# Kernel optimization log

Hardware: AMD Instinct MI355X
Metric: run time of the kernel (lower is better)

## Reference

```python
import jax, jax.numpy as jnp
import numpy as np

B, C, H, W = 8, 256, 64, 64
R = 16  # reduction
D = C // R  # qk dim = 16


def setup_inputs() -> dict:
    key = jax.random.key(0)
    ks = jax.random.split(key, 6)
    s = 1.0 / np.sqrt(C)
    return {
        "x": jax.random.normal(ks[0], (B, C, H, W), jnp.float32),
        "Wq": jax.random.normal(ks[1], (D, C), jnp.float32) * s,
        "bq": jnp.zeros((D,), jnp.float32),
        "Wk": jax.random.normal(ks[2], (D, C), jnp.float32) * s,
        "bk": jnp.zeros((D,), jnp.float32),
        "Wv": jax.random.normal(ks[3], (C, C), jnp.float32) * s,
        "bv": jnp.zeros((C,), jnp.float32),
        "Wo": jax.random.normal(ks[4], (C, C), jnp.float32) * s,
        "bo": jnp.zeros((C,), jnp.float32),
        "gamma": jnp.ones((1,), jnp.float32) * 0.1,
    }


def reference(x, Wq, bq, Wk, bk, Wv, bv, Wo, bo, gamma):
    b, c, h, w = x.shape
    n = h * w
    d = Wq.shape[0]
    scale = d ** (-0.5)
    xf = x.reshape(b, c, n)                                  # [B,C,N]
    # 1x1 convs == channelwise linear projections
    q = jnp.einsum('dc,bcn->bnd', Wq, xf) + bq               # [B,N,D] (query permuted)
    k = jnp.einsum('dc,bcn->bdn', Wk, xf) + bk[:, None]      # [B,D,N]
    v = jnp.einsum('ec,bcn->ben', Wv, xf) + bv[:, None]      # [B,C,N]
    attn = jnp.einsum('bnd,bdm->bnm', q, k) * scale          # [B,N,N]
    attn = jnp.clip(attn, -50.0, 50.0)
    attn = jax.nn.softmax(attn, axis=-1)
    out = jnp.einsum('ben,bmn->bem', v, attn)                # value @ attn^T -> [B,C,N]
    out = jnp.einsum('fc,bcn->bfn', Wo, out) + bo[:, None]   # conv_out
    out = out.reshape(b, c, h, w)
    g = jnp.clip(gamma, 0.0, 1.0)
    return g[0] * out + x
```

## Files before the change

kernel.cpp:

```cpp
#include <hip/hip_runtime.h>
#include <hip/hip_bf16.h>

#define DEVI __device__ __forceinline__

using f32x4  = __attribute__((ext_vector_type(4))) float;
using s16x8  = __attribute__((ext_vector_type(8))) short;
using bf16x8 = __attribute__((ext_vector_type(8))) __bf16;

constexpr int kB = 8;
constexpr int kC = 256;
constexpr int kN = 4096;
constexpr int kD = 16;

DEVI unsigned short f2bf(float f) {
  __hip_bfloat16 h = __float2bfloat16(f);
  return __builtin_bit_cast(unsigned short, h);
}
DEVI s16x8 ld16g(const unsigned short* p) { return *reinterpret_cast<const s16x8*>(p); }
DEVI s16x8 ld16l(const char* b, int off) { return *reinterpret_cast<const s16x8*>(b + off); }
DEVI void  st16l(char* b, int off, s16x8 v) { *reinterpret_cast<s16x8*>(b + off) = v; }
DEVI f32x4 mfma16(s16x8 a, s16x8 bb, f32x4 c) {
  return __builtin_amdgcn_mfma_f32_16x16x32_bf16(
      __builtin_bit_cast(bf16x8, a), __builtin_bit_cast(bf16x8, bb), c, 0, 0, 0);
}
DEVI void gload_lds16(const void* g, void* l) {
  __builtin_amdgcn_global_load_lds((const __attribute__((address_space(1))) void*)g,
                                   (__attribute__((address_space(3))) void*)l, 16, 0, 0);
}

__global__ __launch_bounds__(256) void k_cvt_w(
    const float* wq, const float* wk, const float* wv, const float* wo,
    unsigned short* wqb, unsigned short* wkb, unsigned short* wvb, unsigned short* wob) {
  int i = blockIdx.x * 256 + threadIdx.x;
  if (i < 4096)        wqb[i]         = f2bf(wq[i]);
  else if (i < 8192)   wkb[i - 4096]  = f2bf(wk[i - 4096]);
  else if (i < 73728)  wvb[i - 8192]  = f2bf(wv[i - 8192]);
  else if (i < 139264) wob[i - 73728] = f2bf(wo[i - 73728]);
}

__global__ __launch_bounds__(256) void k_xpose(const float* __restrict__ x,
                                               unsigned short* __restrict__ xbT) {
  __shared__ float tile[64][68];
  int b = blockIdx.z, c0 = blockIdx.y * 64, n0 = blockIdx.x * 64;
  int t = threadIdx.x;
  const float* xp = x + ((size_t)b * kC + c0) * kN + n0;
#pragma unroll
  for (int i = 0; i < 4; i++) {
    int c_l = (t >> 4) + i * 16, n_l = (t & 15) * 4;
    float4 v = *reinterpret_cast<const float4*>(xp + (size_t)c_l * kN + n_l);
    *reinterpret_cast<float4*>(&tile[c_l][n_l]) = v;
  }
  __syncthreads();
  unsigned short* op = xbT + ((size_t)b * kN + n0) * kC + c0;
#pragma unroll
  for (int i = 0; i < 4; i++) {
    int n_l = (t >> 4) + i * 16, c_l = (t & 15) * 4;
    ushort4 u;
    u.x = f2bf(tile[c_l + 0][n_l]);
    u.y = f2bf(tile[c_l + 1][n_l]);
    u.z = f2bf(tile[c_l + 2][n_l]);
    u.w = f2bf(tile[c_l + 3][n_l]);
    *reinterpret_cast<ushort4*>(op + (size_t)n_l * kC + c_l) = u;
  }
}

__global__ __launch_bounds__(256) void k_proj_qkv(
    const unsigned short* __restrict__ xbT,
    const unsigned short* __restrict__ wqb, const unsigned short* __restrict__ wkb,
    const unsigned short* __restrict__ wvb,
    const float* __restrict__ bq, const float* __restrict__ bk, const float* __restrict__ bv,
    unsigned short* __restrict__ qb, unsigned short* __restrict__ kb,
    unsigned short* __restrict__ vt) {
  __shared__ char xlds[64 * 512];
  int b = blockIdx.y, n0 = blockIdx.x * 64;
  int t = threadIdx.x, lane = t & 63, w = t >> 6;
  int r = lane & 15, g = lane >> 4;
  const unsigned short* xp = xbT + ((size_t)b * kN + n0) * kC;
#pragma unroll
  for (int i = 0; i < 8; i++) {
    int ch = i * 256 + t;
    int n_l = ch >> 5, c8 = (ch & 31) << 3;
    s16x8 v = ld16g(xp + (size_t)n_l * kC + c8);
    int off = (n_l << 9) + (c8 << 1);
    off ^= (n_l & 7) << 4;
    st16l(xlds, off, v);
  }
  __syncthreads();
  {
    f32x4 aq = {0.f, 0.f, 0.f, 0.f}, ak = {0.f, 0.f, 0.f, 0.f};
#pragma unroll
    for (int kt2 = 0; kt2 < 8; kt2++) {
      int arow = w * 16 + r;
      int off = (arow << 9) + ((kt2 * 32 + g * 8) << 1);
      off ^= (arow & 7) << 4;
      s16x8 a = ld16l(xlds, off);
      s16x8 bqf = ld16g(wqb + r * kC + kt2 * 32 + g * 8);
      s16x8 bkf = ld16g(wkb + r * kC + kt2 * 32 + g * 8);
      aq = mfma16(a, bqf, aq);
      ak = mfma16(a, bkf, ak);
    }
    int d = r;
    float bqd = bq[d], bkd = bk[d];
    unsigned short* qo = qb + ((size_t)b * kN + n0 + w * 16) * kD + d;
    unsigned short* ko = kb + ((size_t)b * kN + n0 + w * 16) * kD + d;
#pragma unroll
    for (int j = 0; j < 4; j++) {
      int row = g * 4 + j;
      qo[row * kD] = f2bf((aq[j] + bqd) * 0.25f);
      ko[row * kD] = f2bf(ak[j] + bkd);
    }
  }
  {
    f32x4 acc[4][4];
#pragma unroll
    for (int p = 0; p < 4; p++)
#pragma unroll
      for (int np = 0; np < 4; np++) acc[p][np] = f32x4{0.f, 0.f, 0.f, 0.f};
#pragma unroll
    for (int kt2 = 0; kt2 < 8; kt2++) {
      s16x8 af[4], bf_[4];
#pragma unroll
      for (int p = 0; p < 4; p++) {
        int e = w * 64 + p * 16 + r;
        af[p] = ld16g(wvb + (size_t)e * kC + kt2 * 32 + g * 8);
      }
#pragma unroll
      for (int np = 0; np < 4; np++) {
        int nrow = np * 16 + r;
        int off = (nrow << 9) + ((kt2 * 32 + g * 8) << 1);
        off ^= (nrow & 7) << 4;
        bf_[np] = ld16l(xlds, off);
      }
#pragma unroll
      for (int p = 0; p < 4; p++)
#pragma unroll
        for (int np = 0; np < 4; np++) acc[p][np] = mfma16(af[p], bf_[np], acc[p][np]);
    }
#pragma unroll
    for (int p = 0; p < 4; p++) {
#pragma unroll
      for (int j = 0; j < 4; j++) {
        int e = w * 64 + p * 16 + g * 4 + j;
        float bve = bv[e];
        unsigned short* vo = vt + ((size_t)b * kC + e) * kN + n0;
#pragma unroll
        for (int np = 0; np < 4; np++) vo[np * 16 + r] = f2bf(acc[p][np][j] + bve);
      }
    }
  }
}

__global__ __launch_bounds__(256) void k_attn(
    const unsigned short* __restrict__ qb, const unsigned short* __restrict__ kb,
    const unsigned short* __restrict__ vt, const unsigned short* __restrict__ wob,
    const float* __restrict__ bo, const float* __restrict__ gamma,
    const float* __restrict__ x, float* __restrict__ out) {
  __shared__ char smem[73728];
  char* plds = smem + 65536;
  int b = blockIdx.x & 7, q0 = (blockIdx.x >> 3) * 64;
  int t = threadIdx.x, lane = t & 63, w = t >> 6;
  int r = lane & 15, g = lane >> 4;
  const s16x8 z8 = {0, 0, 0, 0, 0, 0, 0, 0};
  s16x8 qf = z8;
  if (g < 2) qf = ld16g(qb + ((size_t)b * kN + q0 + w * 16 + r) * kD + g * 8);
  f32x4 accO[16];
#pragma unroll
  for (int i = 0; i < 16; i++) accO[i] = f32x4{0.f, 0.f, 0.f, 0.f};
  float m = -1e30f, lsum = 0.f;
  const unsigned short* vbase = vt + (size_t)b * kC * kN;
  const unsigned short* kbase = kb + (size_t)b * kN * kD;

  int voff[8];
#pragma unroll
  for (int i = 0; i < 8; i++) {
    int ch = (w * 8 + i) * 64 + lane;
    int e = ch >> 3, kc = ch & 7;
    voff[i] = e * kN + (kc ^ (e & 7)) * 8;
  }
  int koff[4];
#pragma unroll
  for (int nk = 0; nk < 4; nk++) koff[nk] = (nk * 16 + r) * kD + g * 8;

  auto stage_v = [&](int key0, char* buf) {
#pragma unroll
    for (int i = 0; i < 8; i++)
      gload_lds16(vbase + voff[i] + key0, buf + (w * 8 + i) * 1024);
  };

  stage_v(0, smem);
  s16x8 kf_cur[4] = {z8, z8, z8, z8};
  if (g < 2)
#pragma unroll
    for (int nk = 0; nk < 4; nk++) kf_cur[nk] = ld16g(kbase + koff[nk]);

  for (int kt = 0; kt < kN / 64; kt++) {
    char* vbuf = smem + ((kt & 1) << 15);
    __syncthreads();
    if (kt + 1 < kN / 64) stage_v((kt + 1) * 64, smem + (((kt + 1) & 1) << 15));
    s16x8 kf_nxt[4] = {z8, z8, z8, z8};
    if (kt + 1 < kN / 64 && g < 2)
#pragma unroll
      for (int nk = 0; nk < 4; nk++)
        kf_nxt[nk] = ld16g(kbase + (kt + 1) * 64 * kD + koff[nk]);

    f32x4 s[4];
#pragma unroll
    for (int nk = 0; nk < 4; nk++) {
      f32x4 z = {0.f, 0.f, 0.f, 0.f};
      s[nk] = mfma16(kf_cur[nk], qf, z);
    }
#pragma unroll
    for (int nk = 0; nk < 4; nk++)
#pragma unroll
      for (int j = 0; j < 4; j++) s[nk][j] = fminf(50.f, fmaxf(-50.f, s[nk][j]));
    float mx0 = fmaxf(fmaxf(s[0][0], s[0][1]), fmaxf(s[0][2], s[0][3]));
    float mx1 = fmaxf(fmaxf(s[1][0], s[1][1]), fmaxf(s[1][2], s[1][3]));
    float mx2 = fmaxf(fmaxf(s[2][0], s[2][1]), fmaxf(s[2][2], s[2][3]));
    float mx3 = fmaxf(fmaxf(s[3][0], s[3][1]), fmaxf(s[3][2], s[3][3]));
    float mx = fmaxf(fmaxf(mx0, mx1), fmaxf(mx2, mx3));
    mx = fmaxf(mx, __shfl_xor(mx, 16));
    mx = fmaxf(mx, __shfl_xor(mx, 32));
    float mn = fmaxf(m, mx);
    float fs = __expf(m - mn);
    bool need = (mn != m);
    m = mn;
#pragma unroll
    for (int nk = 0; nk < 4; nk++)
#pragma unroll
      for (int j = 0; j < 4; j++) s[nk][j] = __expf(s[nk][j] - mn);
    float sm0 = (s[0][0] + s[0][1]) + (s[0][2] + s[0][3]);
    float sm1 = (s[1][0] + s[1][1]) + (s[1][2] + s[1][3]);
    float sm2 = (s[2][0] + s[2][1]) + (s[2][2] + s[2][3]);
    float sm3 = (s[3][0] + s[3][1]) + (s[3][2] + s[3][3]);
    lsum = lsum * fs + ((sm0 + sm1) + (sm2 + sm3));
#pragma unroll
    for (int nk = 0; nk < 4; nk++) {
      unsigned p01 = (unsigned)f2bf(s[nk][0]) | ((unsigned)f2bf(s[nk][1]) << 16);
      unsigned p23 = (unsigned)f2bf(s[nk][2]) | ((unsigned)f2bf(s[nk][3]) << 16);
      int off = (r << 7) + ((nk * 32 + g * 8) ^ ((r & 7) << 4));
      *reinterpret_cast<uint2*>(plds + w * 2048 + off) = make_uint2(p01, p23);
    }
    if (__any(need)) {
#pragma unroll
      for (int ep = 0; ep < 16; ep++)
#pragma unroll
        for (int j = 0; j < 4; j++) accO[ep][j] *= fs;
    }
    s16x8 pa[2];
#pragma unroll
    for (int h = 0; h < 2; h++) {
      int off = (r << 7) + ((h * 64 + g * 16) ^ ((r & 7) << 4));
      pa[h] = ld16l(plds + w * 2048, off);
    }
    __builtin_amdgcn_s_setprio(1);
#pragma unroll
    for (int ep = 0; ep < 16; ep++) {
#pragma unroll
      for (int h = 0; h < 2; h++) {
        int e = ep * 16 + r;
        int off = (e << 7) + ((h * 64 + g * 16) ^ ((e & 7) << 4));
        s16x8 vb = ld16l(vbuf, off);
        accO[ep] = mfma16(vb, pa[h], accO[ep]);
      }
    }
    __builtin_amdgcn_s_setprio(0);
#pragma unroll
    for (int nk = 0; nk < 4; nk++) kf_cur[nk] = kf_nxt[nk];
  }
  lsum += __shfl_xor(lsum, 16);
  lsum += __shfl_xor(lsum, 32);
  float inv = 1.f / lsum;
  __syncthreads();
  char* alds = smem;
#pragma unroll
  for (int ep = 0; ep < 16; ep++)
#pragma unroll
    for (int j = 0; j < 4; j++) {
      int qrow = w * 16 + r;
      int e = ep * 16 + g * 4 + j;
      int off = (qrow << 9) + ((e << 1) ^ ((qrow & 7) << 4));
      *reinterpret_cast<unsigned short*>(alds + off) = f2bf(accO[ep][j] * inv);
    }
  __syncthreads();
  f32x4 acc2[4][4];
#pragma unroll
  for (int p = 0; p < 4; p++)
#pragma unroll
    for (int np = 0; np < 4; np++) acc2[p][np] = f32x4{0.f, 0.f, 0.f, 0.f};
#pragma unroll
  for (int kt2 = 0; kt2 < 8; kt2++) {
    s16x8 af[4], bf_[4];
#pragma unroll
    for (int p = 0; p < 4; p++) {
      int f = w * 64 + p * 16 + r;
      af[p] = ld16g(wob + (size_t)f * kC + kt2 * 32 + g * 8);
    }
#pragma unroll
    for (int np = 0; np < 4; np++) {
      int mrow = np * 16 + r;
      int off = (mrow << 9) + (((kt2 * 32 + g * 8) << 1) ^ ((mrow & 7) << 4));
      bf_[np] = ld16l(alds, off);
    }
#pragma unroll
    for (int p = 0; p < 4; p++)
#pragma unroll
      for (int np = 0; np < 4; np++) acc2[p][np] = mfma16(af[p], bf_[np], acc2[p][np]);
  }
  float gm = fminf(1.f, fmaxf(0.f, gamma[0]));
#pragma unroll
  for (int p = 0; p < 4; p++) {
#pragma unroll
    for (int j = 0; j < 4; j++) {
      int f = w * 64 + p * 16 + g * 4 + j;
      float bof = bo[f];
      const float* xr = x + ((size_t)b * kC + f) * kN + q0;
      float* orow = out + ((size_t)b * kC + f) * kN + q0;
#pragma unroll
      for (int np = 0; np < 4; np++) {
        int mi = np * 16 + r;
        orow[mi] = gm * (acc2[p][np][j] + bof) + xr[mi];
      }
    }
  }
}

extern "C" void kernel_launch(void* const* d_in, const int* in_sizes, int n_in,
                              void* d_out, int out_size, void* d_ws, size_t ws_size,
                              hipStream_t stream) {
  const float* x     = (const float*)d_in[0];
  const float* Wq    = (const float*)d_in[1];
  const float* bq    = (const float*)d_in[2];
  const float* Wk    = (const float*)d_in[3];
  const float* bk    = (const float*)d_in[4];
  const float* Wv    = (const float*)d_in[5];
  const float* bv    = (const float*)d_in[6];
  const float* Wo    = (const float*)d_in[7];
  const float* bo    = (const float*)d_in[8];
  const float* gamma = (const float*)d_in[9];
  float* out = (float*)d_out;

  unsigned short* xbT = (unsigned short*)d_out;

  char* ws = (char*)d_ws;
  unsigned short* vtb = (unsigned short*)ws; ws += (size_t)kB * kC * kN * 2;
  unsigned short* qb  = (unsigned short*)ws; ws += (size_t)kB * kN * kD * 2;
  unsigned short* kbp = (unsigned short*)ws; ws += (size_t)kB * kN * kD * 2;
  unsigned short* wqb = (unsigned short*)ws; ws += kD * kC * 2;
  unsigned short* wkb = (unsigned short*)ws; ws += kD * kC * 2;
  unsigned short* wvb = (unsigned short*)ws; ws += kC * kC * 2;
  unsigned short* wob = (unsigned short*)ws; ws += kC * kC * 2;

  k_cvt_w<<<dim3(544), dim3(256), 0, stream>>>(Wq, Wk, Wv, Wo, wqb, wkb, wvb, wob);
  k_xpose<<<dim3(kN / 64, kC / 64, kB), dim3(256), 0, stream>>>(x, xbT);
  k_proj_qkv<<<dim3(kN / 64, kB), dim3(256), 0, stream>>>(xbT, wqb, wkb, wvb,
                                                          bq, bk, bv, qb, kbp, vtb);
  k_attn<<<dim3(kN / 64 * kB), dim3(256), 0, stream>>>(qb, kbp, vtb, wob,
                                                       bo, gamma, x, out);
}
```

Baseline: 253.9 us.

## Drop online softmax max with fixed exp2 offset and re-split PV work across waves

Folds log2(e) into the Q scale and replaces the running-max online softmax with a fixed offset (MFMA accumulator initialised to -kM) and clamped exp2. This removes the per-tile max reduction, shuffles and accumulator rescaling. It relies on the score clip at ±50 so the exponentials cannot overflow. The PV stage is also re-partitioned: each wave now owns 64 output channels across all 64 queries instead of 16 queries across all channels. That needs an extra barrier per tile to share P through LDS and per-row inverse sums in LDS. Packed bf16 conversion instructions replace the scalar conversions.

```diff
diff --git a/kernel.cpp b/kernel.cpp
--- a/kernel.cpp
+++ b/kernel.cpp
@@ -12,9 +12,20 @@
 constexpr int kN = 4096;
 constexpr int kD = 16;
 
+#if __has_builtin(__builtin_amdgcn_exp2f)
+#define EXP2(x) __builtin_amdgcn_exp2f(x)
+#else
+#define EXP2(x) exp2f(x)
+#endif
+
 DEVI unsigned short f2bf(float f) {
   __hip_bfloat16 h = __float2bfloat16(f);
   return __builtin_bit_cast(unsigned short, h);
+}
+DEVI unsigned cvtpk(float lo, float hi) {
+  unsigned r;
+  asm("v_cvt_pk_bf16_f32 %0, %1, %2" : "=v"(r) : "v"(lo), "v"(hi));
+  return r;
 }
 DEVI s16x8 ld16g(const unsigned short* p) { return *reinterpret_cast<const s16x8*>(p); }
 DEVI s16x8 ld16l(const char* b, int off) { return *reinterpret_cast<const s16x8*>(b + off); }
@@ -106,7 +117,7 @@
 #pragma unroll
     for (int j = 0; j < 4; j++) {
       int row = g * 4 + j;
-      qo[row * kD] = f2bf((aq[j] + bqd) * 0.25f);
+      qo[row * kD] = f2bf((aq[j] + bqd) * 0.3606737602f);
       ko[row * kD] = f2bf(ak[j] + bkd);
     }
   }
@@ -155,18 +166,26 @@
     const unsigned short* __restrict__ vt, const unsigned short* __restrict__ wob,
     const float* __restrict__ bo, const float* __restrict__ gamma,
     const float* __restrict__ x, float* __restrict__ out) {
-  __shared__ char smem[73728];
+  __shared__ char smem[73984];
   char* plds = smem + 65536;
+  float* linv = reinterpret_cast<float*>(smem + 73728);
   int b = blockIdx.x & 7, q0 = (blockIdx.x >> 3) * 64;
   int t = threadIdx.x, lane = t & 63, w = t >> 6;
   int r = lane & 15, g = lane >> 4;
   const s16x8 z8 = {0, 0, 0, 0, 0, 0, 0, 0};
+  constexpr int NT = kN / 64;
+  constexpr float kM  = 17.3123405f;
+  constexpr float kLo = -89.4470925f;
+  constexpr float kHi = 54.8224115f;
+
   s16x8 qf = z8;
   if (g < 2) qf = ld16g(qb + ((size_t)b * kN + q0 + w * 16 + r) * kD + g * 8);
-  f32x4 accO[16];
-#pragma unroll
-  for (int i = 0; i < 16; i++) accO[i] = f32x4{0.f, 0.f, 0.f, 0.f};
-  float m = -1e30f, lsum = 0.f;
+  f32x4 accO[4][4];
+#pragma unroll
+  for (int ef = 0; ef < 4; ef++)
+#pragma unroll
+    for (int qg = 0; qg < 4; qg++) accO[ef][qg] = f32x4{0.f, 0.f, 0.f, 0.f};
+  float lsum = 0.f;
   const unsigned short* vbase = vt + (size_t)b * kC * kN;
   const unsigned short* kbase = kb + (size_t)b * kN * kD;
 
@@ -180,6 +199,11 @@
   int koff[4];
 #pragma unroll
   for (int nk = 0; nk < 4; nk++) koff[nk] = (nk * 16 + r) * kD + g * 8;
+  const int swz = (r & 7) << 4;
+  const int vE0 = ((w * 64 + r) << 7) + ((g * 16) ^ swz);
+  const int vE1 = ((w * 64 + r) << 7) + ((64 + g * 16) ^ swz);
+  const int pa0 = (r << 7) + ((g * 16) ^ swz);
+  const int pa1 = (r << 7) + ((64 + g * 16) ^ swz);
 
   auto stage_v = [&](int key0, char* buf) {
 #pragma unroll
@@ -193,74 +217,58 @@
 #pragma unroll
     for (int nk = 0; nk < 4; nk++) kf_cur[nk] = ld16g(kbase + koff[nk]);
 
-  for (int kt = 0; kt < kN / 64; kt++) {
+  const f32x4 cini = {-kM, -kM, -kM, -kM};
+  for (int kt = 0; kt < NT; kt++) {
     char* vbuf = smem + ((kt & 1) << 15);
     __syncthreads();
-    if (kt + 1 < kN / 64) stage_v((kt + 1) * 64, smem + (((kt + 1) & 1) << 15));
     s16x8 kf_nxt[4] = {z8, z8, z8, z8};
-    if (kt + 1 < kN / 64 && g < 2)
-#pragma unroll
-      for (int nk = 0; nk < 4; nk++)
-        kf_nxt[nk] = ld16g(kbase + (kt + 1) * 64 * kD + koff[nk]);
+    if (kt + 1 < NT) {
+      stage_v((kt + 1) * 64, smem + (((kt + 1) & 1) << 15));
+      if (g < 2)
+#pragma unroll
+        for (int nk = 0; nk < 4; nk++)
+          kf_nxt[nk] = ld16g(kbase + (kt + 1) * 64 * kD + koff[nk]);
+    }
 
     f32x4 s[4];
 #pragma unroll
-    for (int nk = 0; nk < 4; nk++) {
-      f32x4 z = {0.f, 0.f, 0.f, 0.f};
-      s[nk] = mfma16(kf_cur[nk], qf, z);
-    }
+    for (int nk = 0; nk < 4; nk++) s[nk] = mfma16(kf_cur[nk], qf, cini);
 #pragma unroll
     for (int nk = 0; nk < 4; nk++)
 #pragma unroll
-      for (int j = 0; j < 4; j++) s[nk][j] = fminf(50.f, fmaxf(-50.f, s[nk][j]));
-    float mx0 = fmaxf(fmaxf(s[0][0], s[0][1]), fmaxf(s[0][2], s[0][3]));
-    float mx1 = fmaxf(fmaxf(s[1][0], s[1][1]), fmaxf(s[1][2], s[1][3]));
-    float mx2 = fmaxf(fmaxf(s[2][0], s[2][1]), fmaxf(s[2][2], s[2][3]));
-    float mx3 = fmaxf(fmaxf(s[3][0], s[3][1]), fmaxf(s[3][2], s[3][3]));
-    float mx = fmaxf(fmaxf(mx0, mx1), fmaxf(mx2, mx3));
-    mx = fmaxf(mx, __shfl_xor(mx, 16));
-    mx = fmaxf(mx, __shfl_xor(mx, 32));
-    float mn = fmaxf(m, mx);
-    float fs = __expf(m - mn);
-    bool need = (mn != m);
-    m = mn;
-#pragma unroll
-    for (int nk = 0; nk < 4; nk++)
-#pragma unroll
-      for (int j = 0; j < 4; j++) s[nk][j] = __expf(s[nk][j] - mn);
+      for (int j = 0; j < 4; j++)
+        s[nk][j] = EXP2(fminf(kHi, fmaxf(kLo, s[nk][j])));
     float sm0 = (s[0][0] + s[0][1]) + (s[0][2] + s[0][3]);
     float sm1 = (s[1][0] + s[1][1]) + (s[1][2] + s[1][3]);
     float sm2 = (s[2][0] + s[2][1]) + (s[2][2] + s[2][3]);
     float sm3 = (s[3][0] + s[3][1]) + (s[3][2] + s[3][3]);
-    lsum = lsum * fs + ((sm0 + sm1) + (sm2 + sm3));
+    lsum += (sm0 + sm1) + (sm2 + sm3);
 #pragma unroll
     for (int nk = 0; nk < 4; nk++) {
-      unsigned p01 = (unsigned)f2bf(s[nk][0]) | ((unsigned)f2bf(s[nk][1]) << 16);
-      unsigned p23 = (unsigned)f2bf(s[nk][2]) | ((unsigned)f2bf(s[nk][3]) << 16);
-      int off = (r << 7) + ((nk * 32 + g * 8) ^ ((r & 7) << 4));
-      *reinterpret_cast<uint2*>(plds + w * 2048 + off) = make_uint2(p01, p23);
-    }
-    if (__any(need)) {
-#pragma unroll
-      for (int ep = 0; ep < 16; ep++)
-#pragma unroll
-        for (int j = 0; j < 4; j++) accO[ep][j] *= fs;
-    }
-    s16x8 pa[2];
-#pragma unroll
-    for (int h = 0; h < 2; h++) {
-      int off = (r << 7) + ((h * 64 + g * 16) ^ ((r & 7) << 4));
-      pa[h] = ld16l(plds + w * 2048, off);
+      uint2 pk;
+      pk.x = cvtpk(s[nk][0], s[nk][1]);
+      pk.y = cvtpk(s[nk][2], s[nk][3]);
+      int off = (r << 7) + ((nk * 32 + g * 8) ^ swz);
+      *reinterpret_cast<uint2*>(plds + w * 2048 + off) = pk;
+    }
+    asm volatile("s_waitcnt lgkmcnt(0)" ::: "memory");
+    __builtin_amdgcn_s_barrier();
+
+    s16x8 pa[4][2];
+#pragma unroll
+    for (int qg = 0; qg < 4; qg++) {
+      pa[qg][0] = ld16l(plds, qg * 2048 + pa0);
+      pa[qg][1] = ld16l(plds, qg * 2048 + pa1);
     }
     __builtin_amdgcn_s_setprio(1);
 #pragma unroll
-    for (int ep = 0; ep < 16; ep++) {
-#pragma unroll
-      for (int h = 0; h < 2; h++) {
-        int e = ep * 16 + r;
-        int off = (e << 7) + ((h * 64 + g * 16) ^ ((e & 7) << 4));
-        s16x8 vb = ld16l(vbuf, off);
-        accO[ep] = mfma16(vb, pa[h], accO[ep]);
+    for (int ef = 0; ef < 4; ef++) {
+      s16x8 vb0 = ld16l(vbuf, vE0 + ef * 2048);
+      s16x8 vb1 = ld16l(vbuf, vE1 + ef * 2048);
+#pragma unroll
+      for (int qg = 0; qg < 4; qg++) {
+        accO[ef][qg] = mfma16(vb0, pa[qg][0], accO[ef][qg]);
+        accO[ef][qg] = mfma16(vb1, pa[qg][1], accO[ef][qg]);
       }
     }
     __builtin_amdgcn_s_setprio(0);
@@ -270,16 +278,22 @@
   lsum += __shfl_xor(lsum, 16);
   lsum += __shfl_xor(lsum, 32);
   float inv = 1.f / lsum;
+  if (g == 0) linv[w * 16 + r] = inv;
   __syncthreads();
+  float inv4[4];
+#pragma unroll
+  for (int qg = 0; qg < 4; qg++) inv4[qg] = linv[qg * 16 + r];
   char* alds = smem;
 #pragma unroll
-  for (int ep = 0; ep < 16; ep++)
-#pragma unroll
-    for (int j = 0; j < 4; j++) {
-      int qrow = w * 16 + r;
-      int e = ep * 16 + g * 4 + j;
-      int off = (qrow << 9) + ((e << 1) ^ ((qrow & 7) << 4));
-      *reinterpret_cast<unsigned short*>(alds + off) = f2bf(accO[ep][j] * inv);
+  for (int ef = 0; ef < 4; ef++)
+#pragma unroll
+    for (int qg = 0; qg < 4; qg++) {
+      uint2 pk;
+      pk.x = cvtpk(accO[ef][qg][0] * inv4[qg], accO[ef][qg][1] * inv4[qg]);
+      pk.y = cvtpk(accO[ef][qg][2] * inv4[qg], accO[ef][qg][3] * inv4[qg]);
+      int qrow = qg * 16 + r;
+      int off = (qrow << 9) + ((w * 128 + ef * 32 + g * 8) ^ ((r & 7) << 4));
+      *reinterpret_cast<uint2*>(alds + off) = pk;
     }
   __syncthreads();
   f32x4 acc2[4][4];
```

New measurement: 232.2 us. 1.09x faster.
